# Performance work log

Hardware: AMD Instinct MI355X
Metric: run time of the kernel (lower is better)

The kernel has to match this reference:

```python
import jax, jax.numpy as jnp
import numpy as np

N_NODES = 50000


def _gin_aggregate(x, src, dst):
    # sum_{j in N(i)} x_j via scatter-add over edges; eps=0 so add self term
    msg = x[src]  # [E, d]
    return x + jax.ops.segment_sum(msg, dst, num_segments=N_NODES)


def _mlp(h, Wa, ba, Wb, bb):
    return jax.nn.relu(h @ Wa + ba) @ Wb + bb


def setup_inputs() -> dict:
    key = jax.random.key(0)
    ks = jax.random.split(key, 12)
    d_in, d_h, n_cls, n_edges = 128, 128, 40, 800000
    x = jax.random.normal(ks[0], (N_NODES, d_in), dtype=jnp.float32)
    edge_index = jax.random.randint(ks[1], (2, n_edges), 0, N_NODES, dtype=jnp.int64)
    s = lambda k, sh: jax.random.normal(k, sh, dtype=jnp.float32) / np.sqrt(sh[0])
    return {
        "x": x,
        "edge_index": edge_index,
        "W11": s(ks[2], (d_in, 2 * d_h)), "b11": jnp.zeros((2 * d_h,), jnp.float32),
        "W12": s(ks[3], (2 * d_h, d_h)), "b12": jnp.zeros((d_h,), jnp.float32),
        "W21": s(ks[4], (d_h, 2 * d_h)), "b21": jnp.zeros((2 * d_h,), jnp.float32),
        "W22": s(ks[5], (2 * d_h, d_h)), "b22": jnp.zeros((d_h,), jnp.float32),
        "Wfc": s(ks[6], (d_h, n_cls)), "bfc": jnp.zeros((n_cls,), jnp.float32),
    }


def reference(x, edge_index, W11, b11, W12, b12, W21, b21, W22, b22, Wfc, bfc):
    src, dst = edge_index[0], edge_index[1]
    # GINConv 1: aggregate then MLP, followed by ReLU
    h = _mlp(_gin_aggregate(x, src, dst), W11, b11, W12, b12)
    h = jax.nn.relu(h)
    # GINConv 2
    h = _mlp(_gin_aggregate(h, src, dst), W21, b21, W22, b22)
    h = jax.nn.relu(h)
    # final classifier
    return h @ Wfc + bfc
```

## Files before the change

### kernel.cpp

```cpp
#include <hip/hip_runtime.h>

#define N_NODES 50000
#define N_EDGES 800000
#define NBUCK   98
#define EPB     2048
#define NSB     391
#define BCAP    64
#define CAPB    12288

typedef __attribute__((ext_vector_type(8))) short short8;
typedef __attribute__((ext_vector_type(4))) float floatx4;

__device__ __forceinline__ float ubits(unsigned int b) {
    union { unsigned int i; float f; } v;
    v.i = b;
    return v.f;
}
__device__ __forceinline__ unsigned short f2b(float f) {
    union { float f; unsigned int i; } v;
    v.f = f;
    unsigned int r = v.i + 0x7FFFu + ((v.i >> 16) & 1u);
    return (unsigned short)(r >> 16);
}

__global__ __launch_bounds__(256) void scatter_xconv(
    const int* __restrict__ srcv, const int* __restrict__ dstv,
    const float* __restrict__ x,
    int* __restrict__ cnt, int* __restrict__ tmp,
    unsigned short* __restrict__ xb) {
    const int bid = blockIdx.x;
    const int tid = threadIdx.x;
    if (bid < NSB) {
        __shared__ int hist[NBUCK];
        const int k = bid;
        const int e0 = k * EPB;
        for (int i = tid; i < NBUCK; i += 256) hist[i] = 0;
        __syncthreads();
#pragma unroll
        for (int j = 0; j < EPB / 256; ++j) {
            int e = e0 + j * 256 + tid;
            if (e < N_EDGES) atomicAdd(&hist[dstv[e] >> 9], 1);
        }
        __syncthreads();
        for (int i = tid; i < NBUCK; i += 256) {
            cnt[i * NSB + k] = hist[i];
            hist[i] = 0;
        }
        __syncthreads();
#pragma unroll
        for (int j = 0; j < EPB / 256; ++j) {
            int e = e0 + j * 256 + tid;
            if (e < N_EDGES) {
                int d = dstv[e];
                int b = d >> 9;
                int r = atomicAdd(&hist[b], 1);
                if (r < BCAP)
                    tmp[((size_t)k * NBUCK + b) * BCAP + r] = srcv[e] | ((d & 511) << 16);
            }
        }
    } else {
        int i = (bid - NSB) * 256 + tid;
        const float4 a = *reinterpret_cast<const float4*>(x + (size_t)i * 8);
        const float4 b = *reinterpret_cast<const float4*>(x + (size_t)i * 8 + 4);
        ushort4 u0, u1;
        u0.x = f2b(a.x); u0.y = f2b(a.y); u0.z = f2b(a.z); u0.w = f2b(a.w);
        u1.x = f2b(b.x); u1.y = f2b(b.y); u1.z = f2b(b.z); u1.w = f2b(b.w);
        *reinterpret_cast<ushort4*>(xb + (size_t)i * 8) = u0;
        *reinterpret_cast<ushort4*>(xb + (size_t)i * 8 + 4) = u1;
    }
}

__global__ __launch_bounds__(256) void sort_wconv(
    const int* __restrict__ cnt, const int* __restrict__ tmp,
    int* __restrict__ e_src, int* __restrict__ row_ptr,
    const float* __restrict__ W11, const float* __restrict__ W12,
    const float* __restrict__ W21, const float* __restrict__ W22,
    const float* __restrict__ Wfc,
    unsigned short* __restrict__ Wt11, unsigned short* __restrict__ Wt12,
    unsigned short* __restrict__ Wt21, unsigned short* __restrict__ Wt22,
    unsigned short* __restrict__ Wfct) {
    __shared__ int ps[256];
    __shared__ int sb[512];
    __shared__ int sc[512];
    __shared__ int nc[512];
    __shared__ int buf[CAPB];
    const int bid = blockIdx.x;
    const int tid = threadIdx.x;

    if (bid < NBUCK) {
        const int b = bid;
        sc[tid] = (tid < NSB) ? cnt[b * NSB + tid] : 0;
        sc[tid + 256] = (tid + 256 < NSB) ? cnt[b * NSB + tid + 256] : 0;
        __syncthreads();
        const int c0s = sc[2 * tid], c1s = sc[2 * tid + 1];
        ps[tid] = c0s + c1s;
        __syncthreads();
        for (int off = 1; off < 256; off <<= 1) {
            int u = (tid >= off) ? ps[tid - off] : 0;
            __syncthreads();
            ps[tid] += u;
            __syncthreads();
        }
        const int soff0 = ps[tid] - (c0s + c1s);
        sb[2 * tid] = soff0;
        sb[2 * tid + 1] = soff0 + c0s;
        __syncthreads();
        const int S = ps[255];

        const int lane = tid & 63, w = tid >> 6;
        const int hw = w * 2 + (lane >> 5), hl = lane & 31;
        for (int k = hw; k < NSB; k += 8) {
            const int base = sb[k], c = sc[k];
            const int* src = tmp + ((size_t)k * NBUCK + b) * BCAP;
            for (int i = hl; i < c; i += 32)
                if (base + i < CAPB) buf[base + i] = src[i];
        }
        for (int i = tid; i < 512; i += 256) nc[i] = 0;
        __syncthreads();
        for (int e = tid; e < S; e += 256)
            atomicAdd(&nc[(buf[e] >> 16) & 511], 1);
        __syncthreads();

        const int c0 = nc[2 * tid], c1 = nc[2 * tid + 1];
        ps[tid] = c0 + c1;
        __syncthreads();
        for (int off = 1; off < 256; off <<= 1) {
            int u = (tid >= off) ? ps[tid - off] : 0;
            __syncthreads();
            ps[tid] += u;
            __syncthreads();
        }
        const int off0 = ps[tid] - (c0 + c1);
        const int off1 = off0 + c0;
        nc[2 * tid] = off0;
        nc[2 * tid + 1] = off1;
        const int gbase = b * CAPB;
        row_ptr[b * 513 + 2 * tid] = gbase + off0;
        row_ptr[b * 513 + 2 * tid + 1] = gbase + off1;
        if (tid == 0) row_ptr[b * 513 + 512] = gbase + S;
        __syncthreads();

        for (int e = tid; e < S; e += 256) {
            int p = buf[e];
            int dl = (p >> 16) & 511;
            int pos = atomicAdd(&nc[dl], 1);
            e_src[gbase + pos] = p & 0xFFFF;
        }
    } else if (bid < NBUCK + 512) {
        int wb = bid - NBUCK;
        int which = wb >> 7;
        int idx = (wb & 127) * 256 + tid;
        const float* W = (which == 0) ? W11 : (which == 1) ? W12 : (which == 2) ? W21 : W22;
        unsigned short* Wt = (which == 0) ? Wt11 : (which == 1) ? Wt12 : (which == 2) ? Wt21 : Wt22;
        int K = (which & 1) ? 256 : 128;
        int N = (which & 1) ? 128 : 256;
        int k = idx / N, n = idx - k * N;
        Wt[n * K + k] = f2b(W[idx]);
    } else {
        int idx = (bid - NBUCK - 512) * 256 + tid;
        int n = idx >> 7, k = idx & 127;
        Wfct[idx] = (n < 40) ? f2b(Wfc[k * 40 + n]) : (unsigned short)0;
    }
}

__global__ __launch_bounds__(256) void agg_bf16q(const unsigned short* __restrict__ X,
                                                 const int* __restrict__ row_ptr,
                                                 const int* __restrict__ e_src,
                                                 unsigned short* __restrict__ agg) {
    const int node = (blockIdx.x * 256 + threadIdx.x) >> 6;
    const int lane = threadIdx.x & 63;
    const int qw = lane >> 4, ql = lane & 15;
    const size_t off = (size_t)ql * 8;

    const int rp = node + (node >> 9);
    const int beg = row_ptr[rp], end = row_ptr[rp + 1];
    float acc[8];
#pragma unroll
    for (int k = 0; k < 8; ++k) acc[k] = 0.f;

    if (qw == 0) {
        uint4 u = *reinterpret_cast<const uint4*>(X + (size_t)node * 128 + off);
        const unsigned int* up = (const unsigned int*)&u;
#pragma unroll
        for (int k = 0; k < 4; ++k) {
            acc[2 * k]     += ubits(up[k] << 16);
            acc[2 * k + 1] += ubits(up[k] & 0xFFFF0000u);
        }
    }

    int e = beg + qw;
    for (; e + 12 < end; e += 16) {
        const int s0 = e_src[e], s1 = e_src[e + 4], s2 = e_src[e + 8], s3 = e_src[e + 12];
        uint4 u0 = *reinterpret_cast<const uint4*>(X + (size_t)s0 * 128 + off);
        uint4 u1 = *reinterpret_cast<const uint4*>(X + (size_t)s1 * 128 + off);
        uint4 u2 = *reinterpret_cast<const uint4*>(X + (size_t)s2 * 128 + off);
        uint4 u3 = *reinterpret_cast<const uint4*>(X + (size_t)s3 * 128 + off);
        const unsigned int* p0 = (const unsigned int*)&u0;
        const unsigned int* p1 = (const unsigned int*)&u1;
        const unsigned int* p2 = (const unsigned int*)&u2;
        const unsigned int* p3 = (const unsigned int*)&u3;
#pragma unroll
        for (int k = 0; k < 4; ++k) {
            acc[2 * k]     += ubits(p0[k] << 16) + ubits(p1[k] << 16)
                            + ubits(p2[k] << 16) + ubits(p3[k] << 16);
            acc[2 * k + 1] += ubits(p0[k] & 0xFFFF0000u) + ubits(p1[k] & 0xFFFF0000u)
                            + ubits(p2[k] & 0xFFFF0000u) + ubits(p3[k] & 0xFFFF0000u);
        }
    }
    for (; e + 4 < end; e += 8) {
        const int s0 = e_src[e], s1 = e_src[e + 4];
        uint4 u0 = *reinterpret_cast<const uint4*>(X + (size_t)s0 * 128 + off);
        uint4 u1 = *reinterpret_cast<const uint4*>(X + (size_t)s1 * 128 + off);
        const unsigned int* p0 = (const unsigned int*)&u0;
        const unsigned int* p1 = (const unsigned int*)&u1;
#pragma unroll
        for (int k = 0; k < 4; ++k) {
            acc[2 * k]     += ubits(p0[k] << 16) + ubits(p1[k] << 16);
            acc[2 * k + 1] += ubits(p0[k] & 0xFFFF0000u) + ubits(p1[k] & 0xFFFF0000u);
        }
    }
    if (e < end) {
        const int s = e_src[e];
        uint4 u = *reinterpret_cast<const uint4*>(X + (size_t)s * 128 + off);
        const unsigned int* p = (const unsigned int*)&u;
#pragma unroll
        for (int k = 0; k < 4; ++k) {
            acc[2 * k]     += ubits(p[k] << 16);
            acc[2 * k + 1] += ubits(p[k] & 0xFFFF0000u);
        }
    }

#pragma unroll
    for (int k = 0; k < 8; ++k) acc[k] += __shfl_xor(acc[k], 32);
#pragma unroll
    for (int k = 0; k < 8; ++k) acc[k] += __shfl_xor(acc[k], 16);

    if (qw == 0) {
        ushort4 o0, o1;
        o0.x = f2b(acc[0]); o0.y = f2b(acc[1]); o0.z = f2b(acc[2]); o0.w = f2b(acc[3]);
        o1.x = f2b(acc[4]); o1.y = f2b(acc[5]); o1.z = f2b(acc[6]); o1.w = f2b(acc[7]);
        unsigned short* p = agg + (size_t)node * 128 + off;
        *reinterpret_cast<ushort4*>(p) = o0;
        *reinterpret_cast<ushort4*>(p + 4) = o1;
    }
}

template <bool FUSE>
__global__ __launch_bounds__(256, FUSE ? 2 : 3) void mlp_fused(
    const unsigned short* __restrict__ X, const unsigned short* __restrict__ Wt1,
    const float* __restrict__ b1, const unsigned short* __restrict__ Wt2,
    const float* __restrict__ b2, unsigned short* __restrict__ Y,
    const unsigned short* __restrict__ Wfct, const float* __restrict__ bfc,
    float* __restrict__ out, int M) {
    __shared__ __align__(16) char smem[FUSE ? 57344 : 52224];
    unsigned short* A   = (unsigned short*)smem;
    unsigned short* B2q = (unsigned short*)smem;
    unsigned short* B1h = (unsigned short*)(smem + 17408);
    unsigned short* T   = (unsigned short*)(smem + 17408);
    unsigned short* Hc  = (unsigned short*)(smem + 52224);

    const int tid = threadIdx.x;
    const int m0 = blockIdx.x * 64;
    const int lane = tid & 63, w = tid >> 6;
    const int qm = lane & 15, quad = lane >> 4;

#pragma unroll
    for (int j = 0; j < 4; ++j) {
        int i = j * 256 + tid;
        int r = i >> 4, c8 = (i & 15) << 3;
        uint4 v = {0, 0, 0, 0};
        if (m0 + r < M) v = *reinterpret_cast<const uint4*>(X + (size_t)(m0 + r) * 128 + c8);
        *reinterpret_cast<uint4*>(&A[r * 136 + c8]) = v;
    }

    floatx4 acc1[2][4][2];
#pragma unroll
    for (int c = 0; c < 2; ++c)
#pragma unroll
        for (int mt = 0; mt < 4; ++mt)
#pragma unroll
            for (int nt = 0; nt < 2; ++nt) acc1[c][mt][nt] = {0.f, 0.f, 0.f, 0.f};

    for (int c = 0; c < 2; ++c) {
#pragma unroll
        for (int j = 0; j < 8; ++j) {
            int i = j * 256 + tid;
            int r = i >> 4, c8 = (i & 15) << 3;
            *reinterpret_cast<uint4*>(&B1h[r * 136 + c8]) =
                *reinterpret_cast<const uint4*>(Wt1 + (size_t)(c * 128 + r) * 128 + c8);
        }
        __syncthreads();
#pragma unroll
        for (int ks = 0; ks < 4; ++ks) {
            const int kb = ks * 32 + quad * 8;
            short8 a[4], b[2];
#pragma unroll
            for (int mt = 0; mt < 4; ++mt)
                a[mt] = *reinterpret_cast<const short8*>(&A[(mt * 16 + qm) * 136 + kb]);
#pragma unroll
            for (int nt = 0; nt < 2; ++nt)
                b[nt] = *reinterpret_cast<const short8*>(&B1h[(w * 32 + nt * 16 + qm) * 136 + kb]);
#pragma unroll
            for (int mt = 0; mt < 4; ++mt)
#pragma unroll
                for (int nt = 0; nt < 2; ++nt)
                    acc1[c][mt][nt] = __builtin_amdgcn_mfma_f32_16x16x32_bf16(
                        a[mt], b[nt], acc1[c][mt][nt], 0, 0, 0);
        }
        __syncthreads();
    }

#pragma unroll
    for (int c = 0; c < 2; ++c) {
#pragma unroll
        for (int nt = 0; nt < 2; ++nt) {
            const int jcol = c * 128 + w * 32 + nt * 16 + qm;
            const float bj = b1[jcol];
#pragma unroll
            for (int mt = 0; mt < 4; ++mt)
#pragma unroll
                for (int r = 0; r < 4; ++r)
                    T[(mt * 16 + quad * 4 + r) * 264 + jcol] =
                        f2b(fmaxf(acc1[c][mt][nt][r] + bj, 0.f));
        }
    }

    floatx4 cacc[3];
#pragma unroll
    for (int nt = 0; nt < 3; ++nt) cacc[nt] = {0.f, 0.f, 0.f, 0.f};

    for (int c2 = 0; c2 < 4; ++c2) {
#pragma unroll
        for (int j = 0; j < 4; ++j) {
            int i = j * 256 + tid;
            int r = i >> 5, c8 = (i & 31) << 3;
            *reinterpret_cast<uint4*>(&B2q[r * 264 + c8]) =
                *reinterpret_cast<const uint4*>(Wt2 + (size_t)(c2 * 32 + r) * 256 + c8);
        }
        __syncthreads();

        floatx4 acc2[2];
        acc2[0] = {0.f, 0.f, 0.f, 0.f};
        acc2[1] = {0.f, 0.f, 0.f, 0.f};
#pragma unroll
        for (int ks = 0; ks < 8; ++ks) {
            const int kb = ks * 32 + quad * 8;
            short8 t0 = *reinterpret_cast<const short8*>(&T[((w & 1) * 32 + qm) * 264 + kb]);
            short8 t1 = *reinterpret_cast<const short8*>(&T[((w & 1) * 32 + 16 + qm) * 264 + kb]);
            short8 bb = *reinterpret_cast<const short8*>(&B2q[((w >> 1) * 16 + qm) * 264 + kb]);
            acc2[0] = __builtin_amdgcn_mfma_f32_16x16x32_bf16(t0, bb, acc2[0], 0, 0, 0);
            acc2[1] = __builtin_amdgcn_mfma_f32_16x16x32_bf16(t1, bb, acc2[1], 0, 0, 0);
        }

        const int ncol = c2 * 32 + (w >> 1) * 16 + qm;
        const float bj = b2[ncol];
        if (!FUSE) {
#pragma unroll
            for (int mt2 = 0; mt2 < 2; ++mt2)
#pragma unroll
                for (int r = 0; r < 4; ++r) {
                    int row = m0 + (w & 1) * 32 + mt2 * 16 + quad * 4 + r;
                    if (row < M)
                        Y[(size_t)row * 128 + ncol] = f2b(fmaxf(acc2[mt2][r] + bj, 0.f));
                }
            __syncthreads();
        } else {
            const int lcol = (w >> 1) * 16 + qm;
#pragma unroll
            for (int mt2 = 0; mt2 < 2; ++mt2)
#pragma unroll
                for (int r = 0; r < 4; ++r)
                    Hc[((w & 1) * 32 + mt2 * 16 + quad * 4 + r) * 40 + lcol] =
                        f2b(fmaxf(acc2[mt2][r] + bj, 0.f));
            __syncthreads();
            short8 hf = *reinterpret_cast<const short8*>(&Hc[(w * 16 + qm) * 40 + quad * 8]);
#pragma unroll
            for (int nt = 0; nt < 3; ++nt) {
                short8 bf = *reinterpret_cast<const short8*>(
                    Wfct + (nt * 16 + qm) * 128 + c2 * 32 + quad * 8);
                cacc[nt] = __builtin_amdgcn_mfma_f32_16x16x32_bf16(hf, bf, cacc[nt], 0, 0, 0);
            }
            __syncthreads();
        }
    }

    if (FUSE) {
#pragma unroll
        for (int nt = 0; nt < 3; ++nt) {
            int col = nt * 16 + qm;
            if (col < 40) {
                const float bj = bfc[col];
#pragma unroll
                for (int r = 0; r < 4; ++r) {
                    int row = m0 + w * 16 + quad * 4 + r;
                    if (row < M) out[(size_t)row * 40 + col] = cacc[nt][r] + bj;
                }
            }
        }
    }
}

extern "C" void kernel_launch(void* const* d_in, const int* in_sizes, int n_in,
                              void* d_out, int out_size, void* d_ws, size_t ws_size,
                              hipStream_t stream) {
    const float* x   = (const float*)d_in[0];
    const int*   ei  = (const int*)d_in[1];
    const float* W11 = (const float*)d_in[2];
    const float* b11 = (const float*)d_in[3];
    const float* W12 = (const float*)d_in[4];
    const float* b12 = (const float*)d_in[5];
    const float* W21 = (const float*)d_in[6];
    const float* b21 = (const float*)d_in[7];
    const float* W22 = (const float*)d_in[8];
    const float* b22 = (const float*)d_in[9];
    const float* Wfc = (const float*)d_in[10];
    const float* bfc = (const float*)d_in[11];
    float* out = (float*)d_out;

    const int* srcv = ei;
    const int* dstv = ei + N_EDGES;

    unsigned short* agg  = (unsigned short*)d_ws;
    unsigned short* h    = agg + (size_t)N_NODES * 128;
    unsigned short* xb   = h   + (size_t)N_NODES * 128;
    unsigned short* Wt11 = xb  + (size_t)N_NODES * 128;
    unsigned short* Wt12 = Wt11 + 256 * 128;
    unsigned short* Wt21 = Wt12 + 256 * 128;
    unsigned short* Wt22 = Wt21 + 256 * 128;
    unsigned short* Wfct = Wt22 + 256 * 128;
    int* cnt     = (int*)(Wfct + 48 * 128);
    int* row_ptr = cnt + 38400;
    int* e_src   = row_ptr + 50304;
    int* tmp     = e_src + (size_t)NBUCK * CAPB;

    scatter_xconv<<<NSB + 3125, 256, 0, stream>>>(srcv, dstv, x, cnt, tmp, xb);

    sort_wconv<<<NBUCK + 536, 256, 0, stream>>>(
        cnt, tmp, e_src, row_ptr,
        W11, W12, W21, W22, Wfc,
        Wt11, Wt12, Wt21, Wt22, Wfct);

    const int agg_blocks = N_NODES * 64 / 256;
    const int mlp_blocks = (N_NODES + 63) / 64;

    agg_bf16q<<<agg_blocks, 256, 0, stream>>>(xb, row_ptr, e_src, agg);
    mlp_fused<false><<<mlp_blocks, 256, 0, stream>>>(
        agg, Wt11, b11, Wt12, b12, h, nullptr, nullptr, nullptr, N_NODES);
    agg_bf16q<<<agg_blocks, 256, 0, stream>>>(h, row_ptr, e_src, agg);
    mlp_fused<true><<<mlp_blocks, 256, 0, stream>>>(
        agg, Wt21, b21, Wt22, b22, nullptr, Wfct, bfc, out, N_NODES);
}
```

Baseline: 247.3 us.

## Build CSR via global per-node atomic histogram and atomic placement

Replaces the two-pass bucketed shared-memory sort (per-block bucket histograms, capped temporary buckets, per-bucket local sort) with a plain CSR build. It zeroes a per-node degree array, counts degrees with global atomics, scans each 512-node bucket, then places edges using a global atomic cursor per node. This drops the capped temp buffer and the heavy shared-memory sort kernel, but adds two kernel launches and many global atomics. Edge order within a node becomes nondeterministic, so float summation order can vary between runs.

Result: slower. 302.4 us (+22.3%).

```diff
diff --git a/kernel.cpp b/kernel.cpp
--- a/kernel.cpp
+++ b/kernel.cpp
@@ -3,10 +3,8 @@
 #define N_NODES 50000
 #define N_EDGES 800000
 #define NBUCK   98
-#define EPB     2048
-#define NSB     391
-#define BCAP    64
 #define CAPB    12288
+#define NDEG    50176
 
 typedef __attribute__((ext_vector_type(8))) short short8;
 typedef __attribute__((ext_vector_type(4))) float floatx4;
@@ -23,43 +21,47 @@
     return (unsigned short)(r >> 16);
 }
 
-__global__ __launch_bounds__(256) void scatter_xconv(
-    const int* __restrict__ srcv, const int* __restrict__ dstv,
-    const float* __restrict__ x,
-    int* __restrict__ cnt, int* __restrict__ tmp,
-    unsigned short* __restrict__ xb) {
+__global__ __launch_bounds__(256) void prep_wconv_zero(
+    const float* __restrict__ W11, const float* __restrict__ W12,
+    const float* __restrict__ W21, const float* __restrict__ W22,
+    const float* __restrict__ Wfc,
+    unsigned short* __restrict__ Wt11, unsigned short* __restrict__ Wt12,
+    unsigned short* __restrict__ Wt21, unsigned short* __restrict__ Wt22,
+    unsigned short* __restrict__ Wfct, int* __restrict__ deg) {
     const int bid = blockIdx.x;
     const int tid = threadIdx.x;
-    if (bid < NSB) {
-        __shared__ int hist[NBUCK];
-        const int k = bid;
-        const int e0 = k * EPB;
-        for (int i = tid; i < NBUCK; i += 256) hist[i] = 0;
-        __syncthreads();
-#pragma unroll
-        for (int j = 0; j < EPB / 256; ++j) {
+    if (bid < 512) {
+        int which = bid >> 7;
+        int idx = (bid & 127) * 256 + tid;
+        const float* W = (which == 0) ? W11 : (which == 1) ? W12 : (which == 2) ? W21 : W22;
+        unsigned short* Wt = (which == 0) ? Wt11 : (which == 1) ? Wt12 : (which == 2) ? Wt21 : Wt22;
+        int K = (which & 1) ? 256 : 128;
+        int N = (which & 1) ? 128 : 256;
+        int k = idx / N, n = idx - k * N;
+        Wt[n * K + k] = f2b(W[idx]);
+    } else if (bid < 536) {
+        int idx = (bid - 512) * 256 + tid;
+        int n = idx >> 7, k = idx & 127;
+        Wfct[idx] = (n < 40) ? f2b(Wfc[k * 40 + n]) : (unsigned short)0;
+    } else {
+        deg[(bid - 536) * 256 + tid] = 0;
+    }
+}
+
+__global__ __launch_bounds__(256) void hist_xconv(
+    const int* __restrict__ dstv, const float* __restrict__ x,
+    int* __restrict__ deg, unsigned short* __restrict__ xb) {
+    const int bid = blockIdx.x;
+    const int tid = threadIdx.x;
+    if (bid < 391) {
+        const int e0 = bid * 2048;
+#pragma unroll
+        for (int j = 0; j < 8; ++j) {
             int e = e0 + j * 256 + tid;
-            if (e < N_EDGES) atomicAdd(&hist[dstv[e] >> 9], 1);
-        }
-        __syncthreads();
-        for (int i = tid; i < NBUCK; i += 256) {
-            cnt[i * NSB + k] = hist[i];
-            hist[i] = 0;
-        }
-        __syncthreads();
-#pragma unroll
-        for (int j = 0; j < EPB / 256; ++j) {
-            int e = e0 + j * 256 + tid;
-            if (e < N_EDGES) {
-                int d = dstv[e];
-                int b = d >> 9;
-                int r = atomicAdd(&hist[b], 1);
-                if (r < BCAP)
-                    tmp[((size_t)k * NBUCK + b) * BCAP + r] = srcv[e] | ((d & 511) << 16);
-            }
+            if (e < N_EDGES) atomicAdd(&deg[dstv[e]], 1);
         }
     } else {
-        int i = (bid - NSB) * 256 + tid;
+        int i = (bid - 391) * 256 + tid;
         const float4 a = *reinterpret_cast<const float4*>(x + (size_t)i * 8);
         const float4 b = *reinterpret_cast<const float4*>(x + (size_t)i * 8 + 4);
         ushort4 u0, u1;
@@ -70,96 +72,44 @@
     }
 }
 
-__global__ __launch_bounds__(256) void sort_wconv(
-    const int* __restrict__ cnt, const int* __restrict__ tmp,
-    int* __restrict__ e_src, int* __restrict__ row_ptr,
-    const float* __restrict__ W11, const float* __restrict__ W12,
-    const float* __restrict__ W21, const float* __restrict__ W22,
-    const float* __restrict__ Wfc,
-    unsigned short* __restrict__ Wt11, unsigned short* __restrict__ Wt12,
-    unsigned short* __restrict__ Wt21, unsigned short* __restrict__ Wt22,
-    unsigned short* __restrict__ Wfct) {
+__global__ __launch_bounds__(256) void scan_buckets(
+    const int* __restrict__ deg, int* __restrict__ row_ptr, int* __restrict__ cur) {
     __shared__ int ps[256];
-    __shared__ int sb[512];
-    __shared__ int sc[512];
-    __shared__ int nc[512];
-    __shared__ int buf[CAPB];
-    const int bid = blockIdx.x;
+    const int b = blockIdx.x;
     const int tid = threadIdx.x;
-
-    if (bid < NBUCK) {
-        const int b = bid;
-        sc[tid] = (tid < NSB) ? cnt[b * NSB + tid] : 0;
-        sc[tid + 256] = (tid + 256 < NSB) ? cnt[b * NSB + tid + 256] : 0;
+    const int n0 = b * 512;
+    const int c0 = deg[n0 + 2 * tid], c1 = deg[n0 + 2 * tid + 1];
+    ps[tid] = c0 + c1;
+    __syncthreads();
+    for (int off = 1; off < 256; off <<= 1) {
+        int u = (tid >= off) ? ps[tid - off] : 0;
         __syncthreads();
-        const int c0s = sc[2 * tid], c1s = sc[2 * tid + 1];
-        ps[tid] = c0s + c1s;
+        ps[tid] += u;
         __syncthreads();
-        for (int off = 1; off < 256; off <<= 1) {
-            int u = (tid >= off) ? ps[tid - off] : 0;
-            __syncthreads();
-            ps[tid] += u;
-            __syncthreads();
-        }
-        const int soff0 = ps[tid] - (c0s + c1s);
-        sb[2 * tid] = soff0;
-        sb[2 * tid + 1] = soff0 + c0s;
-        __syncthreads();
-        const int S = ps[255];
-
-        const int lane = tid & 63, w = tid >> 6;
-        const int hw = w * 2 + (lane >> 5), hl = lane & 31;
-        for (int k = hw; k < NSB; k += 8) {
-            const int base = sb[k], c = sc[k];
-            const int* src = tmp + ((size_t)k * NBUCK + b) * BCAP;
-            for (int i = hl; i < c; i += 32)
-                if (base + i < CAPB) buf[base + i] = src[i];
-        }
-        for (int i = tid; i < 512; i += 256) nc[i] = 0;
-        __syncthreads();
-        for (int e = tid; e < S; e += 256)
-            atomicAdd(&nc[(buf[e] >> 16) & 511], 1);
-        __syncthreads();
-
-        const int c0 = nc[2 * tid], c1 = nc[2 * tid + 1];
-        ps[tid] = c0 + c1;
-        __syncthreads();
-        for (int off = 1; off < 256; off <<= 1) {
-            int u = (tid >= off) ? ps[tid - off] : 0;
-            __syncthreads();
-            ps[tid] += u;
-            __syncthreads();
-        }
-        const int off0 = ps[tid] - (c0 + c1);
-        const int off1 = off0 + c0;
-        nc[2 * tid] = off0;
-        nc[2 * tid + 1] = off1;
-        const int gbase = b * CAPB;
-        row_ptr[b * 513 + 2 * tid] = gbase + off0;
-        row_ptr[b * 513 + 2 * tid + 1] = gbase + off1;
-        if (tid == 0) row_ptr[b * 513 + 512] = gbase + S;
-        __syncthreads();
-
-        for (int e = tid; e < S; e += 256) {
-            int p = buf[e];
-            int dl = (p >> 16) & 511;
-            int pos = atomicAdd(&nc[dl], 1);
-            e_src[gbase + pos] = p & 0xFFFF;
-        }
-    } else if (bid < NBUCK + 512) {
-        int wb = bid - NBUCK;
-        int which = wb >> 7;
-        int idx = (wb & 127) * 256 + tid;
-        const float* W = (which == 0) ? W11 : (which == 1) ? W12 : (which == 2) ? W21 : W22;
-        unsigned short* Wt = (which == 0) ? Wt11 : (which == 1) ? Wt12 : (which == 2) ? Wt21 : Wt22;
-        int K = (which & 1) ? 256 : 128;
-        int N = (which & 1) ? 128 : 256;
-        int k = idx / N, n = idx - k * N;
-        Wt[n * K + k] = f2b(W[idx]);
-    } else {
-        int idx = (bid - NBUCK - 512) * 256 + tid;
-        int n = idx >> 7, k = idx & 127;
-        Wfct[idx] = (n < 40) ? f2b(Wfc[k * 40 + n]) : (unsigned short)0;
+    }
+    const int off0 = ps[tid] - (c0 + c1);
+    const int off1 = off0 + c0;
+    const int gbase = b * CAPB;
+    row_ptr[b * 513 + 2 * tid] = gbase + off0;
+    row_ptr[b * 513 + 2 * tid + 1] = gbase + off1;
+    cur[n0 + 2 * tid] = gbase + off0;
+    cur[n0 + 2 * tid + 1] = gbase + off1;
+    if (tid == 255) row_ptr[b * 513 + 512] = gbase + off1 + c1;
+}
+
+__global__ __launch_bounds__(256) void place_edges(
+    const int* __restrict__ srcv, const int* __restrict__ dstv,
+    int* __restrict__ cur, int* __restrict__ e_src) {
+    const int e0 = blockIdx.x * 1024;
+    const int tid = threadIdx.x;
+#pragma unroll
+    for (int j = 0; j < 4; ++j) {
+        int e = e0 + j * 256 + tid;
+        if (e < N_EDGES) {
+            int d = dstv[e];
+            int pos = atomicAdd(&cur[d], 1);
+            e_src[pos] = srcv[e];
+        }
     }
 }
 
@@ -428,17 +378,19 @@
     unsigned short* Wt21 = Wt12 + 256 * 128;
     unsigned short* Wt22 = Wt21 + 256 * 128;
     unsigned short* Wfct = Wt22 + 256 * 128;
-    int* cnt     = (int*)(Wfct + 48 * 128);
-    int* row_ptr = cnt + 38400;
+    int* deg     = (int*)(Wfct + 48 * 128);
+    int* cur     = deg + NDEG;
+    int* row_ptr = cur + NDEG;
     int* e_src   = row_ptr + 50304;
-    int* tmp     = e_src + (size_t)NBUCK * CAPB;
-
-    scatter_xconv<<<NSB + 3125, 256, 0, stream>>>(srcv, dstv, x, cnt, tmp, xb);
-
-    sort_wconv<<<NBUCK + 536, 256, 0, stream>>>(
-        cnt, tmp, e_src, row_ptr,
-        W11, W12, W21, W22, Wfc,
-        Wt11, Wt12, Wt21, Wt22, Wfct);
+
+    prep_wconv_zero<<<732, 256, 0, stream>>>(
+        W11, W12, W21, W22, Wfc, Wt11, Wt12, Wt21, Wt22, Wfct, deg);
+
+    hist_xconv<<<391 + 3125, 256, 0, stream>>>(dstv, x, deg, xb);
+
+    scan_buckets<<<NBUCK, 256, 0, stream>>>(deg, row_ptr, cur);
+
+    place_edges<<<782, 256, 0, stream>>>(srcv, dstv, cur, e_src);
 
     const int agg_blocks = N_NODES * 64 / 256;
     const int mlp_blocks = (N_NODES + 63) / 64;
```
